# Performance work log

Hardware: AMD Instinct MI355X
Metric: run time of the kernel (lower is better)

## Reference

```python
import jax, jax.numpy as jnp
import numpy as np

L = 9  # local window size


def local_windows(x, l):
    # x: (n, c, h, w) -> (n, c, l*l, h, w): all l*l shifted views (zero-padded),
    # equivalent to F.unfold(x, kernel=(l,l), stride=1, padding=l//2).
    n, c, h, w = x.shape
    pad = l // 2
    xp = jnp.pad(x, ((0, 0), (0, 0), (pad, pad), (pad, pad)))
    views = [xp[:, :, i:i + h, j:j + w] for i in range(l) for j in range(l)]
    return jnp.stack(views, axis=2)


def setup_inputs() -> dict:
    key = jax.random.key(0)
    k1, k2, k3 = jax.random.split(key, 3)
    n, c, h, w = 2, 128, 64, 64
    ft = jax.random.normal(k1, (n, c, h, w), dtype=jnp.float32)
    fk = jax.random.normal(k2, (n, c, h, w), dtype=jnp.float32)
    # 1x1 conv weight shared between key and query projections: (out_c, in_c)
    W = jax.random.normal(k3, (128, 128), dtype=jnp.float32) * (1.0 / np.sqrt(128))
    return {"ft": ft, "fk": fk, "W": W}


def reference(ft, fk, W):
    # 1x1 conv == channel matmul
    key = jnp.einsum('oi,nihw->nohw', W, ft)    # key from frame t
    query = jnp.einsum('oi,nihw->nohw', W, fk)  # query from frame k
    # f_similar(query, key, L): per-pixel query dotted with L*L local keys
    key_win = local_windows(key, L)             # (n, c, L*L, h, w)
    sim = jnp.einsum('nchw,nckhw->nhwk', query, key_win)  # (n, h, w, L*L)
    weight = jax.nn.softmax(sim, axis=-1)
    # f_weighting(ft, weight, L): weighted sum of L*L local raw-ft vectors
    ft_win = local_windows(ft, L)                # (n, c, L*L, h, w)
    out = jnp.einsum('nckhw,nhwk->nchw', ft_win, weight)
    return out
```

## Files before the change

### kernel.cpp

```cpp
#include <hip/hip_runtime.h>
#include <hip/hip_bf16.h>


#define Hh 64
#define Ww 64
#define Cc 128
#define Nn 2
#define HW (Hh * Ww)
#define CHW (Cc * HW)

typedef _Float16 h8 __attribute__((ext_vector_type(8)));
typedef _Float16 h4 __attribute__((ext_vector_type(4)));
typedef float f4v __attribute__((ext_vector_type(4)));

#ifndef __has_builtin
#define __has_builtin(x) 0
#endif

#if __has_builtin(__builtin_amdgcn_ds_read_tr16_b64_v4f16)
#define TR_BUILTIN 1
typedef __fp16 g4 __attribute__((__vector_size__(4 * sizeof(__fp16))));
static __device__ __forceinline__ h4 tr16(const _Float16* p) {
    g4 r = __builtin_amdgcn_ds_read_tr16_b64_v4f16(
        (__attribute__((address_space(3))) g4*)p);
    return __builtin_bit_cast(h4, r);
}
#else
#define TR_BUILTIN 0
static __device__ __forceinline__ h4 tr16(const _Float16* p) {
    h4 r;
    asm volatile("ds_read_b64_tr_b16 %0, %1"
                 : "=v"(r)
                 : "v"((__attribute__((address_space(3))) _Float16*)p));
    return r;
}
#endif

__global__ __launch_bounds__(256) void proj_kernel(const float* __restrict__ ft,
                                                   const float* __restrict__ fk,
                                                   const float* __restrict__ Wm,
                                                   _Float16* __restrict__ Qbuf,
                                                   _Float16* __restrict__ Kbuf,
                                                   _Float16* __restrict__ fth) {
    __shared__ __align__(16) _Float16 Wth[128 * 136];
    __shared__ __align__(16) _Float16 xkh[16 * 136];
    __shared__ __align__(16) _Float16 xqh[16 * 136];
    const int t = threadIdx.x;
    const int p0 = blockIdx.x * 16;
    const int nn = p0 >> 12;
    const int gbase = nn * CHW + (p0 & 4095);

#pragma unroll 4
    for (int e = t; e < 4096; e += 256) {
        const int n = e >> 5, ch = e & 31;
        const float4 v = *(const float4*)&Wm[n * 128 + (ch << 2)];
        h4 hv; hv[0] = (_Float16)v.x; hv[1] = (_Float16)v.y;
               hv[2] = (_Float16)v.z; hv[3] = (_Float16)v.w;
        *(h4*)&Wth[n * 136 + (ch << 2)] = hv;
    }
#pragma unroll
    for (int e = t; e < 512; e += 256) {
        const int c = e >> 2, pc = e & 3;
        const float4 vk = *(const float4*)&ft[gbase + c * HW + (pc << 2)];
        const float4 vq = *(const float4*)&fk[gbase + c * HW + (pc << 2)];
        const int px = pc << 2;
        xkh[(px    ) * 136 + c] = (_Float16)vk.x;
        xkh[(px + 1) * 136 + c] = (_Float16)vk.y;
        xkh[(px + 2) * 136 + c] = (_Float16)vk.z;
        xkh[(px + 3) * 136 + c] = (_Float16)vk.w;
        xqh[(px    ) * 136 + c] = (_Float16)vq.x;
        xqh[(px + 1) * 136 + c] = (_Float16)vq.y;
        xqh[(px + 2) * 136 + c] = (_Float16)vq.z;
        xqh[(px + 3) * 136 + c] = (_Float16)vq.w;
    }
    __syncthreads();

    {
        const int px = t >> 4, cq = t & 15;
        *(h8*)&fth[(size_t)(p0 + px) * 128 + (cq << 3)] =
            *(const h8*)&xkh[px * 136 + (cq << 3)];
    }

    const int lane = t & 63, wv = t >> 6;
    const int quad = lane >> 4, l15 = lane & 15;
    const _Float16* xs = (wv >> 1) ? xqh : xkh;
    _Float16* dst = (wv >> 1) ? Qbuf : Kbuf;
    const int nt0 = (wv & 1) << 2;
    const int abase = l15 * 136 + (quad << 3);
    const h8 a0 = *(const h8*)&xs[abase];
    const h8 a1 = *(const h8*)&xs[abase + 32];
    const h8 a2 = *(const h8*)&xs[abase + 64];
    const h8 a3 = *(const h8*)&xs[abase + 96];
#pragma unroll
    for (int ni = 0; ni < 4; ++ni) {
        const int nt = nt0 + ni;
        const int bbase = (nt * 16 + l15) * 136 + (quad << 3);
        const h8 b0 = *(const h8*)&Wth[bbase];
        const h8 b1 = *(const h8*)&Wth[bbase + 32];
        const h8 b2 = *(const h8*)&Wth[bbase + 64];
        const h8 b3 = *(const h8*)&Wth[bbase + 96];
        f4v acc = {0.f, 0.f, 0.f, 0.f};
        acc = __builtin_amdgcn_mfma_f32_16x16x32_f16(a0, b0, acc, 0, 0, 0);
        acc = __builtin_amdgcn_mfma_f32_16x16x32_f16(a1, b1, acc, 0, 0, 0);
        acc = __builtin_amdgcn_mfma_f32_16x16x32_f16(a2, b2, acc, 0, 0, 0);
        acc = __builtin_amdgcn_mfma_f32_16x16x32_f16(a3, b3, acc, 0, 0, 0);
        const int col = nt * 16 + l15;
        const size_t rb = (size_t)(p0 + (quad << 2)) * 128 + col;
#pragma unroll
        for (int r = 0; r < 4; ++r)
            dst[rb + (size_t)r * 128] = (_Float16)acc[r];
    }
}

#define FTL2 2568
__global__ __launch_bounds__(256, 3) void sim_weight_kernel(const _Float16* __restrict__ Qbuf,
                                                            const _Float16* __restrict__ Kbuf,
                                                            const _Float16* __restrict__ fth,
                                                            float* __restrict__ out) {
    __shared__ __align__(16) unsigned char smem[44192];
    _Float16* Ksw  = (_Float16*)smem;
    _Float16* ftl  = (_Float16*)smem;
    _Float16* simb = (_Float16*)(smem + 41088);
    float*    redM = (float*)(smem + 43680);
    float*    redS = (float*)(smem + 43936);

    const int t  = threadIdx.x;
    const int b  = blockIdx.x;
    const int x0 = (b & 7) << 3;
    const int y0 = ((b >> 3) & 31) << 1;
    const int nn = b >> 8;

#pragma unroll
    for (int i = 0; i < 10; ++i) {
        const int e = t + (i << 8);
        const int v = e >> 4, ci = e & 15;
        const int gx = x0 + (v & 15) - 4;
        const int gy = y0 + (v >> 4) - 4;
        h8 val = {0, 0, 0, 0, 0, 0, 0, 0};
        if ((unsigned)gx < 64u && (unsigned)gy < 64u)
            val = *(const h8*)&Kbuf[(size_t)((nn << 12) + (gy << 6) + gx) * 128 + (ci << 3)];
        *(h8*)&Ksw[(v << 7) + ((ci ^ (v & 15)) << 3)] = val;
    }
    __syncthreads();

    h8 pf[10];
#pragma unroll
    for (int i = 0; i < 10; ++i) {
        const int e = t + (i << 8);
        const int v = e >> 4, ci = e & 15;
        const int gx = x0 + (v & 15) - 4;
        const int gy = y0 + (v >> 4) - 4;
        h8 val = {0, 0, 0, 0, 0, 0, 0, 0};
        if ((unsigned)gx < 64u && (unsigned)gy < 64u)
            val = *(const h8*)&fth[(size_t)((nn << 12) + (gy << 6) + gx) * 128 + (ci << 3)];
        pf[i] = val;
    }

    const int lane = t & 63, wv = t >> 6;
    const int quad = lane >> 4, l15 = lane & 15;
    const int py = l15 >> 3, px = l15 & 7;
    const size_t pgQ = (size_t)((nn << 12) + ((y0 + py) << 6) + x0 + px) * 128;
    f4v sa = {0.f, 0.f, 0.f, 0.f}, sb = sa, sc = sa, sd = sa;
#pragma unroll
    for (int kc = 0; kc < 4; ++kc) {
        const int ci = (kc << 2) + quad;
        const h8 q  = *(const h8*)&Qbuf[pgQ + (ci << 3)];
        const h8 kA = *(const h8*)&Ksw[((((wv    ) << 4) + l15) << 7) + ((ci ^ l15) << 3)];
        const h8 kB = *(const h8*)&Ksw[((((wv + 4) << 4) + l15) << 7) + ((ci ^ l15) << 3)];
        const h8 kC = *(const h8*)&Ksw[((((8     ) << 4) + l15) << 7) + ((ci ^ l15) << 3)];
        const h8 kD = *(const h8*)&Ksw[((((9     ) << 4) + l15) << 7) + ((ci ^ l15) << 3)];
        sa = __builtin_amdgcn_mfma_f32_16x16x32_f16(kA, q, sa, 0, 0, 0);
        sb = __builtin_amdgcn_mfma_f32_16x16x32_f16(kB, q, sb, 0, 0, 0);
        sc = __builtin_amdgcn_mfma_f32_16x16x32_f16(kC, q, sc, 0, 0, 0);
        sd = __builtin_amdgcn_mfma_f32_16x16x32_f16(kD, q, sd, 0, 0, 0);
    }

    float m = -3.0e38f;
#pragma unroll
    for (int reg = 0; reg < 4; ++reg) {
        const int dx = (quad << 2) + reg - px;
        if ((unsigned)dx < 9u) {
            if ((unsigned)(wv - py) < 9u) m = fmaxf(m, sa[reg]);
            m = fmaxf(m, sb[reg]);
            m = fmaxf(m, sc[reg]);
            if (py) m = fmaxf(m, sd[reg]);
        }
    }
    m = fmaxf(m, __shfl_xor(m, 16));
    m = fmaxf(m, __shfl_xor(m, 32));
    if (quad == 0) redM[(wv << 4) + l15] = m;
    __syncthreads();

#pragma unroll
    for (int i = 0; i < 10; ++i) {
        const int e = t + (i << 8);
        const int v = e >> 4, ci = e & 15;
        *(h8*)&ftl[(ci >> 1) * FTL2 + (v << 4) + ((ci & 1) << 3)] = pf[i];
    }

    const float mm = fmaxf(fmaxf(redM[l15], redM[16 + l15]),
                           fmaxf(redM[32 + l15], redM[48 + l15]));
    float ssum = 0.f;
#pragma unroll
    for (int reg = 0; reg < 4; ++reg) {
        const int dx = (quad << 2) + reg - px;
        const bool okx = (unsigned)dx < 9u;
        {
            const int ry = wv - py;
            const bool ok = okx && ((unsigned)ry < 9u);
            const float e = ok ? __expf(sa[reg] - mm) : 0.f;
            if (ok) simb[((ry * 9 + dx) << 4) + l15] = (_Float16)e;
            ssum += e;
        }
        {
            const int ry = wv + 4 - py;
            const float e = okx ? __expf(sb[reg] - mm) : 0.f;
            if (okx) simb[((ry * 9 + dx) << 4) + l15] = (_Float16)e;
            ssum += e;
        }
        {
            const int ry = 8 - py;
            const bool ok = okx && (wv == 0);
            const float e = ok ? __expf(sc[reg] - mm) : 0.f;
            if (ok) simb[((ry * 9 + dx) << 4) + l15] = (_Float16)e;
            ssum += e;
        }
        {
            const bool ok = okx && (wv == 1) && (py == 1);
            const float e = ok ? __expf(sd[reg] - mm) : 0.f;
            if (ok) simb[((8 * 9 + dx) << 4) + l15] = (_Float16)e;
            ssum += e;
        }
    }
    ssum += __shfl_xor(ssum, 16);
    ssum += __shfl_xor(ssum, 32);
    if (quad == 0) redS[(wv << 4) + l15] = ssum;
    __syncthreads();

    const _Float16* ftc0 = ftl + wv * FTL2;
    const _Float16* ftc1 = ftl + (wv + 4) * FTL2;
    h4 bfr[20];
#pragma unroll
    for (int r = 0; r < 10; ++r) {
        bfr[r]      = tr16(ftc0 + (r << 8) + (lane << 2));
        bfr[10 + r] = tr16(ftc1 + (r << 8) + (lane << 2));
    }

#if !TR_BUILTIN
    asm volatile("s_waitcnt lgkmcnt(0)");
    __builtin_amdgcn_sched_barrier(0);
#endif

    f4v aw0 = {0.f, 0.f, 0.f, 0.f}, aw1 = aw0;
#pragma unroll
    for (int r = 0; r < 10; ++r) {
        const int ry = r - py;
        const bool okr = (unsigned)ry < 9u;
        h4 afr;
#pragma unroll
        for (int j = 0; j < 4; ++j) {
            const int dx = (quad << 2) + j - px;
            const bool ok = okr && ((unsigned)dx < 9u);
            afr[j] = ok ? simb[(((ry * 9 + dx) << 4)) + l15] : (_Float16)0.f;
        }
        aw0 = __builtin_amdgcn_mfma_f32_16x16x16f16(afr, bfr[r],      aw0, 0, 0, 0);
        aw1 = __builtin_amdgcn_mfma_f32_16x16x16f16(afr, bfr[10 + r], aw1, 0, 0, 0);
    }

    {
        const int p0q = quad << 2;
        const float iv0 = 1.f / (redS[p0q    ] + redS[16 + p0q    ] + redS[32 + p0q    ] + redS[48 + p0q    ]);
        const float iv1 = 1.f / (redS[p0q + 1] + redS[16 + p0q + 1] + redS[32 + p0q + 1] + redS[48 + p0q + 1]);
        const float iv2 = 1.f / (redS[p0q + 2] + redS[16 + p0q + 2] + redS[32 + p0q + 2] + redS[48 + p0q + 2]);
        const float iv3 = 1.f / (redS[p0q + 3] + redS[16 + p0q + 3] + redS[32 + p0q + 3] + redS[48 + p0q + 3]);
        const int yo = y0 + (p0q >> 3);
        const int xb = (yo << 6) + x0 + (p0q & 7);
        const int c0 = (wv << 4) + l15;
        const int c1 = ((wv + 4) << 4) + l15;
        const size_t ob0 = ((size_t)((nn << 7) + c0) << 12) + xb;
        const size_t ob1 = ((size_t)((nn << 7) + c1) << 12) + xb;
        float4 o0, o1;
        o0.x = aw0[0] * iv0; o0.y = aw0[1] * iv1; o0.z = aw0[2] * iv2; o0.w = aw0[3] * iv3;
        o1.x = aw1[0] * iv0; o1.y = aw1[1] * iv1; o1.z = aw1[2] * iv2; o1.w = aw1[3] * iv3;
        *(float4*)&out[ob0] = o0;
        *(float4*)&out[ob1] = o1;
    }
}

extern "C" void kernel_launch(void* const* d_in, const int* in_sizes, int n_in,
                              void* d_out, int out_size, void* d_ws, size_t ws_size,
                              hipStream_t stream) {
    const float* ft = (const float*)d_in[0];
    const float* fk = (const float*)d_in[1];
    const float* Wm = (const float*)d_in[2];
    float* out = (float*)d_out;

    _Float16* wsh  = (_Float16*)d_ws;
    _Float16* Qbuf = wsh;
    _Float16* Kbuf = wsh + 1048576;
    _Float16* fth  = wsh + 2097152;

    proj_kernel<<<512, 256, 0, stream>>>(ft, fk, Wm, Qbuf, Kbuf, fth);
    sim_weight_kernel<<<512, 256, 0, stream>>>(Qbuf, Kbuf, fth, out);
}
```

Before: 76.93 us.

## Merge projection and similarity kernels with a grid-wide atomic barrier

Fuses the 1x1 projection kernel and the local-attention kernel into one persistent launch. Each block now projects exactly the pixel tile it will later attend over, keeping its query projection in LDS instead of writing it to global memory. Key and raw-ft tiles are still written to global memory, and all blocks meet at a spin-wait atomic counter barrier before neighbouring key windows are read. This removes a kernel launch boundary and the Q global round trip, but adds a memset, a grid barrier that deadlocks unless all 512 blocks are co-resident, and lower occupancy (2 blocks per CU instead of 3) from larger LDS use.

```diff
diff --git a/kernel.cpp b/kernel.cpp
--- a/kernel.cpp
+++ b/kernel.cpp
@@ -8,6 +8,7 @@
 #define Nn 2
 #define HW (Hh * Ww)
 #define CHW (Cc * HW)
+#define NBLK 512u
 
 typedef _Float16 h8 __attribute__((ext_vector_type(8)));
 typedef _Float16 h4 __attribute__((ext_vector_type(4)));
@@ -36,34 +37,50 @@
 }
 #endif
 
-__global__ __launch_bounds__(256) void proj_kernel(const float* __restrict__ ft,
-                                                   const float* __restrict__ fk,
-                                                   const float* __restrict__ Wm,
-                                                   _Float16* __restrict__ Qbuf,
-                                                   _Float16* __restrict__ Kbuf,
-                                                   _Float16* __restrict__ fth) {
-    __shared__ __align__(16) _Float16 Wth[128 * 136];
-    __shared__ __align__(16) _Float16 xkh[16 * 136];
-    __shared__ __align__(16) _Float16 xqh[16 * 136];
-    const int t = threadIdx.x;
-    const int p0 = blockIdx.x * 16;
-    const int nn = p0 >> 12;
-    const int gbase = nn * CHW + (p0 & 4095);
+#define FTL2 2568
+__global__ __launch_bounds__(256, 2) void ila_merged(const float* __restrict__ ft,
+                                                     const float* __restrict__ fk,
+                                                     const float* __restrict__ Wm,
+                                                     _Float16* __restrict__ Kbuf,
+                                                     _Float16* __restrict__ fth,
+                                                     unsigned int* __restrict__ cnt,
+                                                     float* __restrict__ out) {
+    __shared__ __align__(16) unsigned char smem[50976];
+    _Float16* Wth  = (_Float16*)smem;
+    _Float16* xkh  = (_Float16*)(smem + 34816);
+    _Float16* xqh  = (_Float16*)(smem + 39168);
+    _Float16* Ksw  = (_Float16*)smem;
+    _Float16* ftl  = (_Float16*)smem;
+    _Float16* Qlds = (_Float16*)(smem + 43520);
+    _Float16* simb = (_Float16*)(smem + 47872);
+    float*    redM = (float*)(smem + 50464);
+    float*    redS = (float*)(smem + 50720);
+
+    const int t  = threadIdx.x;
+    const int b  = blockIdx.x;
+    const int x0 = (b & 7) << 3;
+    const int y0 = ((b >> 3) & 31) << 1;
+    const int nn = b >> 8;
+
+    const int lane = t & 63, wv = t >> 6;
+    const int quad = lane >> 4, l15 = lane & 15;
 
 #pragma unroll 4
     for (int e = t; e < 4096; e += 256) {
-        const int n = e >> 5, ch = e & 31;
-        const float4 v = *(const float4*)&Wm[n * 128 + (ch << 2)];
+        const int o = e >> 5, ch = e & 31;
+        const float4 v = *(const float4*)&Wm[o * 128 + (ch << 2)];
         h4 hv; hv[0] = (_Float16)v.x; hv[1] = (_Float16)v.y;
                hv[2] = (_Float16)v.z; hv[3] = (_Float16)v.w;
-        *(h4*)&Wth[n * 136 + (ch << 2)] = hv;
+        *(h4*)&Wth[o * 136 + (ch << 2)] = hv;
     }
 #pragma unroll
     for (int e = t; e < 512; e += 256) {
         const int c = e >> 2, pc = e & 3;
-        const float4 vk = *(const float4*)&ft[gbase + c * HW + (pc << 2)];
-        const float4 vq = *(const float4*)&fk[gbase + c * HW + (pc << 2)];
-        const int px = pc << 2;
+        const int py = pc >> 1, xs4 = (pc & 1) << 2;
+        const int ga = nn * CHW + c * HW + ((y0 + py) << 6) + x0 + xs4;
+        const float4 vk = *(const float4*)&ft[ga];
+        const float4 vq = *(const float4*)&fk[ga];
+        const int px = (py << 3) + xs4;
         xkh[(px    ) * 136 + c] = (_Float16)vk.x;
         xkh[(px + 1) * 136 + c] = (_Float16)vk.y;
         xkh[(px + 2) * 136 + c] = (_Float16)vk.z;
@@ -77,58 +94,56 @@
 
     {
         const int px = t >> 4, cq = t & 15;
-        *(h8*)&fth[(size_t)(p0 + px) * 128 + (cq << 3)] =
-            *(const h8*)&xkh[px * 136 + (cq << 3)];
-    }
-
-    const int lane = t & 63, wv = t >> 6;
-    const int quad = lane >> 4, l15 = lane & 15;
-    const _Float16* xs = (wv >> 1) ? xqh : xkh;
-    _Float16* dst = (wv >> 1) ? Qbuf : Kbuf;
-    const int nt0 = (wv & 1) << 2;
-    const int abase = l15 * 136 + (quad << 3);
-    const h8 a0 = *(const h8*)&xs[abase];
-    const h8 a1 = *(const h8*)&xs[abase + 32];
-    const h8 a2 = *(const h8*)&xs[abase + 64];
-    const h8 a3 = *(const h8*)&xs[abase + 96];
-#pragma unroll
-    for (int ni = 0; ni < 4; ++ni) {
-        const int nt = nt0 + ni;
-        const int bbase = (nt * 16 + l15) * 136 + (quad << 3);
-        const h8 b0 = *(const h8*)&Wth[bbase];
-        const h8 b1 = *(const h8*)&Wth[bbase + 32];
-        const h8 b2 = *(const h8*)&Wth[bbase + 64];
-        const h8 b3 = *(const h8*)&Wth[bbase + 96];
-        f4v acc = {0.f, 0.f, 0.f, 0.f};
-        acc = __builtin_amdgcn_mfma_f32_16x16x32_f16(a0, b0, acc, 0, 0, 0);
-        acc = __builtin_amdgcn_mfma_f32_16x16x32_f16(a1, b1, acc, 0, 0, 0);
-        acc = __builtin_amdgcn_mfma_f32_16x16x32_f16(a2, b2, acc, 0, 0, 0);
-        acc = __builtin_amdgcn_mfma_f32_16x16x32_f16(a3, b3, acc, 0, 0, 0);
-        const int col = nt * 16 + l15;
-        const size_t rb = (size_t)(p0 + (quad << 2)) * 128 + col;
-#pragma unroll
-        for (int r = 0; r < 4; ++r)
-            dst[rb + (size_t)r * 128] = (_Float16)acc[r];
-    }
-}
-
-#define FTL2 2568
-__global__ __launch_bounds__(256, 3) void sim_weight_kernel(const _Float16* __restrict__ Qbuf,
-                                                            const _Float16* __restrict__ Kbuf,
-                                                            const _Float16* __restrict__ fth,
-                                                            float* __restrict__ out) {
-    __shared__ __align__(16) unsigned char smem[44192];
-    _Float16* Ksw  = (_Float16*)smem;
-    _Float16* ftl  = (_Float16*)smem;
-    _Float16* simb = (_Float16*)(smem + 41088);
-    float*    redM = (float*)(smem + 43680);
-    float*    redS = (float*)(smem + 43936);
-
-    const int t  = threadIdx.x;
-    const int b  = blockIdx.x;
-    const int x0 = (b & 7) << 3;
-    const int y0 = ((b >> 3) & 31) << 1;
-    const int nn = b >> 8;
+        const size_t gp = (size_t)((nn << 12) + ((y0 + (px >> 3)) << 6) + x0 + (px & 7)) * 128;
+        *(h8*)&fth[gp + (cq << 3)] = *(const h8*)&xkh[px * 136 + (cq << 3)];
+    }
+
+    {
+        const _Float16* xs = (wv >> 1) ? xqh : xkh;
+        const int nt0 = (wv & 1) << 2;
+        const int abase = l15 * 136 + (quad << 3);
+        const h8 a0 = *(const h8*)&xs[abase];
+        const h8 a1 = *(const h8*)&xs[abase + 32];
+        const h8 a2 = *(const h8*)&xs[abase + 64];
+        const h8 a3 = *(const h8*)&xs[abase + 96];
+#pragma unroll
+        for (int ni = 0; ni < 4; ++ni) {
+            const int nt = nt0 + ni;
+            const int bbase = (nt * 16 + l15) * 136 + (quad << 3);
+            const h8 b0 = *(const h8*)&Wth[bbase];
+            const h8 b1 = *(const h8*)&Wth[bbase + 32];
+            const h8 b2 = *(const h8*)&Wth[bbase + 64];
+            const h8 b3 = *(const h8*)&Wth[bbase + 96];
+            f4v acc = {0.f, 0.f, 0.f, 0.f};
+            acc = __builtin_amdgcn_mfma_f32_16x16x32_f16(a0, b0, acc, 0, 0, 0);
+            acc = __builtin_amdgcn_mfma_f32_16x16x32_f16(a1, b1, acc, 0, 0, 0);
+            acc = __builtin_amdgcn_mfma_f32_16x16x32_f16(a2, b2, acc, 0, 0, 0);
+            acc = __builtin_amdgcn_mfma_f32_16x16x32_f16(a3, b3, acc, 0, 0, 0);
+            const int col = nt * 16 + l15;
+            if (wv >> 1) {
+#pragma unroll
+                for (int r = 0; r < 4; ++r)
+                    Qlds[((quad << 2) + r) * 136 + col] = (_Float16)acc[r];
+            } else {
+#pragma unroll
+                for (int r = 0; r < 4; ++r) {
+                    const int p = (quad << 2) + r;
+                    Kbuf[(size_t)((nn << 12) + ((y0 + (p >> 3)) << 6) + x0 + (p & 7)) * 128 + col] =
+                        (_Float16)acc[r];
+                }
+            }
+        }
+    }
+
+    __threadfence();
+    __syncthreads();
+    if (t == 0) {
+        __hip_atomic_fetch_add(cnt, 1u, __ATOMIC_ACQ_REL, __HIP_MEMORY_SCOPE_AGENT);
+        while (__hip_atomic_load(cnt, __ATOMIC_ACQUIRE, __HIP_MEMORY_SCOPE_AGENT) < NBLK)
+            __builtin_amdgcn_s_sleep(2);
+    }
+    __syncthreads();
+    __threadfence();
 
 #pragma unroll
     for (int i = 0; i < 10; ++i) {
@@ -156,23 +171,23 @@
         pf[i] = val;
     }
 
-    const int lane = t & 63, wv = t >> 6;
-    const int quad = lane >> 4, l15 = lane & 15;
     const int py = l15 >> 3, px = l15 & 7;
-    const size_t pgQ = (size_t)((nn << 12) + ((y0 + py) << 6) + x0 + px) * 128;
+    h8 qb[4];
+#pragma unroll
+    for (int kc = 0; kc < 4; ++kc)
+        qb[kc] = *(const h8*)&Qlds[l15 * 136 + (((kc << 2) + quad) << 3)];
     f4v sa = {0.f, 0.f, 0.f, 0.f}, sb = sa, sc = sa, sd = sa;
 #pragma unroll
     for (int kc = 0; kc < 4; ++kc) {
         const int ci = (kc << 2) + quad;
-        const h8 q  = *(const h8*)&Qbuf[pgQ + (ci << 3)];
         const h8 kA = *(const h8*)&Ksw[((((wv    ) << 4) + l15) << 7) + ((ci ^ l15) << 3)];
         const h8 kB = *(const h8*)&Ksw[((((wv + 4) << 4) + l15) << 7) + ((ci ^ l15) << 3)];
         const h8 kC = *(const h8*)&Ksw[((((8     ) << 4) + l15) << 7) + ((ci ^ l15) << 3)];
         const h8 kD = *(const h8*)&Ksw[((((9     ) << 4) + l15) << 7) + ((ci ^ l15) << 3)];
-        sa = __builtin_amdgcn_mfma_f32_16x16x32_f16(kA, q, sa, 0, 0, 0);
-        sb = __builtin_amdgcn_mfma_f32_16x16x32_f16(kB, q, sb, 0, 0, 0);
-        sc = __builtin_amdgcn_mfma_f32_16x16x32_f16(kC, q, sc, 0, 0, 0);
-        sd = __builtin_amdgcn_mfma_f32_16x16x32_f16(kD, q, sd, 0, 0, 0);
+        sa = __builtin_amdgcn_mfma_f32_16x16x32_f16(kA, qb[kc], sa, 0, 0, 0);
+        sb = __builtin_amdgcn_mfma_f32_16x16x32_f16(kB, qb[kc], sb, 0, 0, 0);
+        sc = __builtin_amdgcn_mfma_f32_16x16x32_f16(kC, qb[kc], sc, 0, 0, 0);
+        sd = __builtin_amdgcn_mfma_f32_16x16x32_f16(kD, qb[kc], sd, 0, 0, 0);
     }
 
     float m = -3.0e38f;
@@ -295,11 +310,10 @@
     const float* Wm = (const float*)d_in[2];
     float* out = (float*)d_out;
 
-    _Float16* wsh  = (_Float16*)d_ws;
-    _Float16* Qbuf = wsh;
-    _Float16* Kbuf = wsh + 1048576;
-    _Float16* fth  = wsh + 2097152;
-
-    proj_kernel<<<512, 256, 0, stream>>>(ft, fk, Wm, Qbuf, Kbuf, fth);
-    sim_weight_kernel<<<512, 256, 0, stream>>>(Qbuf, Kbuf, fth, out);
+    _Float16* Kbuf = (_Float16*)d_ws;
+    _Float16* fth  = (_Float16*)d_ws + 1048576;
+    unsigned int* cnt = (unsigned int*)((char*)d_ws + (4u << 20));
+
+    hipMemsetAsync(cnt, 0, 128, stream);
+    ila_merged<<<512, 256, 0, stream>>>(ft, fk, Wm, Kbuf, fth, cnt, out);
 }
```

Result: slower. 189.0 us (+145.7%).
